# Kernel optimization log

Hardware: AMD Instinct MI355X
Metric: run time of the kernel (lower is better)

Reference implementation:

```python
import jax, jax.numpy as jnp
import numpy as np

B, S, D, H = 2, 2048, 1024, 16
DK = D // H  # 64
EPS = 1e-10
ROPE_BASE = 500000.0


def _rms_norm(x, w):
    # RMSNorm over last dim: w * x / sqrt(mean(x^2) + eps)
    return w * x * jax.lax.rsqrt(jnp.mean(x * x, axis=-1, keepdims=True) + EPS)


def _rope_tables(seq_len, dk):
    inv_freq = 1.0 / (ROPE_BASE ** (jnp.arange(0, dk, 2, dtype=jnp.float32) / dk))
    t = jnp.arange(seq_len, dtype=jnp.float32)
    freqs = jnp.outer(t, inv_freq)            # (S, dk/2)
    emb = jnp.concatenate([freqs, freqs], -1)  # (S, dk)
    return jnp.cos(emb), jnp.sin(emb)


def _rotate_half(x):
    x1, x2 = jnp.split(x, 2, axis=-1)
    return jnp.concatenate([-x2, x1], axis=-1)


def setup_inputs() -> dict:
    key = jax.random.key(0)
    ks = jax.random.split(key, 8)
    scale = 1.0 / np.sqrt(D)
    return {
        "q": jax.random.normal(ks[0], (B, S, D), jnp.float32),
        "k": jax.random.normal(ks[1], (B, S, D), jnp.float32),
        "v": jax.random.normal(ks[2], (B, S, D), jnp.float32),
        "Wq": jax.random.normal(ks[3], (D, D), jnp.float32) * scale,
        "Wk": jax.random.normal(ks[4], (D, D), jnp.float32) * scale,
        "Wv": jax.random.normal(ks[5], (D, D), jnp.float32) * scale,
        "Wo": jax.random.normal(ks[6], (D, D), jnp.float32) * scale,
        "q_norm_w": jnp.ones((DK,), jnp.float32) + 0.02 * jax.random.normal(ks[7], (DK,), jnp.float32),
        "k_norm_w": jnp.ones((DK,), jnp.float32),
    }


def reference(q, k, v, Wq, Wk, Wv, Wo, q_norm_w, k_norm_w):
    Bq, Sq, _ = q.shape
    # Projections (torch Linear: x @ W.T), split into heads -> (B, H, S, DK)
    def proj(x, W):
        return (x @ W.T).reshape(Bq, Sq, H, DK).transpose(0, 2, 1, 3)
    query, key_, value = proj(q, Wq), proj(k, Wk), proj(v, Wv)
    # Per-head QK RMSNorm
    query = _rms_norm(query, q_norm_w)
    key_ = _rms_norm(key_, k_norm_w)
    # RoPE
    cos, sin = _rope_tables(Sq, DK)  # (S, DK) each; broadcast over (B, H)
    query = query * cos + _rotate_half(query) * sin
    key_ = key_ * cos + _rotate_half(key_) * sin
    # Causal attention
    scale = 1.0 / np.sqrt(DK)
    scores = jnp.einsum("bhqd,bhkd->bhqk", query, key_) * scale
    causal = jnp.tril(jnp.ones((Sq, Sq), bool))
    scores = jnp.where(causal, scores, -jnp.inf)
    probs = jax.nn.softmax(scores, axis=-1)
    attn = jnp.einsum("bhqk,bhkd->bhqd", probs, value)
    # Merge heads and output projection
    attn = attn.transpose(0, 2, 1, 3).reshape(Bq, Sq, D)
    return attn @ Wo.T
```

## Files before the change

### kernel.cpp

```cpp
#include <hip/hip_runtime.h>
#include <hip/hip_bf16.h>
#include <math.h>

#define B_  2
#define S_  2048
#define D_  1024
#define H_  16
#define DK_ 64

typedef __attribute__((ext_vector_type(8))) short bf16x8;
typedef __attribute__((ext_vector_type(4))) float f32x4;

#define MFMA_BF16(a, b, c) __builtin_amdgcn_mfma_f32_16x16x32_bf16((a), (b), (c), 0, 0, 0)

#define QSCALE 0.18033688011112042f
#define ROPE_L2 0.591611512f

__device__ __forceinline__ unsigned short f2bf(float f) {
  unsigned int u = __float_as_uint(f);
  u += 0x7FFFu + ((u >> 16) & 1u);
  return (unsigned short)(u >> 16);
}

__device__ __forceinline__ void gl_lds16(const void* g, void* l) {
  __builtin_amdgcn_global_load_lds(
      (const __attribute__((address_space(1))) void*)g,
      (__attribute__((address_space(3))) void*)l, 16, 0, 0);
}

__device__ __forceinline__ int lsw(int row, int col) {
  return row * 64 + ((((col) >> 3) ^ (row & 7)) << 3) + (col & 7);
}

__global__ __launch_bounds__(256)
void cvt_bf16(const float* __restrict__ q, const float* __restrict__ k,
              const float* __restrict__ v, const float* __restrict__ wq,
              const float* __restrict__ wk, const float* __restrict__ wv,
              const float* __restrict__ wo,
              unsigned short* __restrict__ qb, unsigned short* __restrict__ kb,
              unsigned short* __restrict__ vb, unsigned short* __restrict__ wqb,
              unsigned short* __restrict__ wkb, unsigned short* __restrict__ wvb,
              unsigned short* __restrict__ wob) {
  const float* src; unsigned short* dst; int n;
  switch (blockIdx.y) {
    case 0: src = q;  dst = qb;  n = B_ * S_ * D_; break;
    case 1: src = k;  dst = kb;  n = B_ * S_ * D_; break;
    case 2: src = v;  dst = vb;  n = B_ * S_ * D_; break;
    case 3: src = wq; dst = wqb; n = D_ * D_; break;
    case 4: src = wk; dst = wkb; n = D_ * D_; break;
    case 5: src = wv; dst = wvb; n = D_ * D_; break;
    default: src = wo; dst = wob; n = D_ * D_; break;
  }
  const int i = (blockIdx.x * 256 + threadIdx.x) * 4;
  if (i >= n) return;
  float4 val = *(const float4*)&src[i];
  ushort4 r4;
  r4.x = f2bf(val.x); r4.y = f2bf(val.y); r4.z = f2bf(val.z); r4.w = f2bf(val.w);
  *(ushort4*)&dst[i] = r4;
}

__global__ __launch_bounds__(256)
void gemm_qkv(const unsigned short* __restrict__ qa, const unsigned short* __restrict__ ka,
              const unsigned short* __restrict__ va,
              const unsigned short* __restrict__ wq, const unsigned short* __restrict__ wk,
              const unsigned short* __restrict__ wv,
              unsigned short* __restrict__ Qo, unsigned short* __restrict__ Ko,
              unsigned short* __restrict__ Vto,
              const float* __restrict__ qnw, const float* __restrict__ knw) {
  __shared__ unsigned short As[2][128 * 32];
  __shared__ unsigned short Bs[2][128 * 32];
  const int z = blockIdx.z;
  const unsigned short* A = (z == 0) ? qa : (z == 1) ? ka : va;
  const unsigned short* W = (z == 0) ? wq : (z == 1) ? wk : wv;

  const int t = threadIdx.x, lane = t & 63, wave = t >> 6;
  const int l16 = lane & 15, quad = lane >> 4;
  const int wm = wave >> 1, wn = wave & 1;
  const int m0 = blockIdx.y * 128, j0 = blockIdx.x * 128;

  f32x4 acc[4][4];
#pragma unroll
  for (int i = 0; i < 4; ++i)
#pragma unroll
    for (int j = 0; j < 4; ++j) acc[i][j] = (f32x4)(0.0f);

  auto stage = [&](int kb, int buf) {
#pragma unroll
    for (int i = 0; i < 2; ++i) {
      const int c  = (wave * 2 + i) * 64 + lane;
      const int r  = c >> 2;
      const int co = (c & 3) * 8;
      gl_lds16(&A[(size_t)(m0 + r) * D_ + kb + co], &As[buf][(wave * 2 + i) * 512]);
      gl_lds16(&W[(size_t)(j0 + r) * D_ + kb + co], &Bs[buf][(wave * 2 + i) * 512]);
    }
  };

  stage(0, 0);
  for (int kb = 0; kb < D_; kb += 32) {
    const int buf = (kb >> 5) & 1;
    __syncthreads();
    if (kb + 32 < D_) stage(kb + 32, buf ^ 1);

    bf16x8 af[4], bfr[4];
#pragma unroll
    for (int mi = 0; mi < 4; ++mi)
      af[mi] = *(const bf16x8*)&As[buf][(wm * 64 + mi * 16 + l16) * 32 + quad * 8];
#pragma unroll
    for (int ni = 0; ni < 4; ++ni)
      bfr[ni] = *(const bf16x8*)&Bs[buf][(wn * 64 + ni * 16 + l16) * 32 + quad * 8];
#pragma unroll
    for (int mi = 0; mi < 4; ++mi)
#pragma unroll
      for (int ni = 0; ni < 4; ++ni)
        acc[mi][ni] = MFMA_BF16(af[mi], bfr[ni], acc[mi][ni]);
  }

  const int h = blockIdx.x * 2 + wn;
  if (z == 2) {
#pragma unroll
    for (int mi = 0; mi < 4; ++mi) {
      const int rowb = m0 + wm * 64 + mi * 16 + quad * 4;
      const int b = rowb >> 11, s0 = rowb & (S_ - 1);
#pragma unroll
      for (int ni = 0; ni < 4; ++ni) {
        const int dk = ni * 16 + l16;
        const unsigned int u0 =
            (unsigned int)f2bf(acc[mi][ni][0]) | ((unsigned int)f2bf(acc[mi][ni][1]) << 16);
        const unsigned int u1 =
            (unsigned int)f2bf(acc[mi][ni][2]) | ((unsigned int)f2bf(acc[mi][ni][3]) << 16);
        *(uint2*)&Vto[((size_t)((b * H_ + h) * DK_ + dk)) * S_ + s0] = make_uint2(u0, u1);
      }
    }
  } else {
    unsigned short* out = (z == 0) ? Qo : Ko;
    const float* nw = (z == 0) ? qnw : knw;
    const float sc  = (z == 0) ? QSCALE : 1.0f;
    float wv_[4];
#pragma unroll
    for (int ni = 0; ni < 4; ++ni) wv_[ni] = nw[ni * 16 + l16];
    const float invA = exp2f(-(float)l16 * ROPE_L2);
    const float invB = exp2f(-(float)(16 + l16) * ROPE_L2);
#pragma unroll
    for (int mi = 0; mi < 4; ++mi) {
#pragma unroll
      for (int r = 0; r < 4; ++r) {
        const int rowg = m0 + wm * 64 + mi * 16 + quad * 4 + r;
        const int b = rowg >> 11, s = rowg & (S_ - 1);
        float ss = 0.f;
#pragma unroll
        for (int ni = 0; ni < 4; ++ni) ss += acc[mi][ni][r] * acc[mi][ni][r];
#pragma unroll
        for (int m = 1; m < 16; m <<= 1) ss += __shfl_xor(ss, m);
        const float rms = rsqrtf(ss * (1.0f / DK_) + 1e-10f);
        float xn[4];
#pragma unroll
        for (int ni = 0; ni < 4; ++ni) xn[ni] = wv_[ni] * acc[mi][ni][r] * rms;
        const float fA = (float)s * invA, fB = (float)s * invB;
        const float cA = __cosf(fA) * sc, sA = __sinf(fA) * sc;
        const float cB = __cosf(fB) * sc, sB = __sinf(fB) * sc;
        float o0 = xn[0] * cA - xn[2] * sA;
        float o1 = xn[1] * cB - xn[3] * sB;
        float o2 = xn[2] * cA + xn[0] * sA;
        float o3 = xn[3] * cB + xn[1] * sB;
        const size_t base = ((size_t)(b * H_ + h) * S_ + s) * DK_;
        out[base +  0 + l16] = f2bf(o0);
        out[base + 16 + l16] = f2bf(o1);
        out[base + 32 + l16] = f2bf(o2);
        out[base + 48 + l16] = f2bf(o3);
      }
    }
  }
}

__global__ __launch_bounds__(256)
void flash3(const unsigned short* __restrict__ Q, const unsigned short* __restrict__ K,
            const unsigned short* __restrict__ Vt, unsigned short* __restrict__ Oa) {
  __shared__ unsigned short Ks[2][64 * 64];
  __shared__ unsigned short Vs[2][64 * 64];
  __shared__ unsigned short Ps[64 * 64];
  const int bx = blockIdx.x;
  const int idx = bx >> 5;
  const int qt = (idx < 16) ? idx : (47 - idx);
  const int bh = bx & 31;
  const int t = threadIdx.x, lane = t & 63, wave = t >> 6;
  const int l16 = lane & 15, quad = lane >> 4;
  const size_t hb = (size_t)bh * S_ * DK_;
  const unsigned short* Qh  = Q + hb;
  const unsigned short* Kh  = K + hb;
  const unsigned short* Vth = Vt + hb;

  bf16x8 qf[2];
#pragma unroll
  for (int ks = 0; ks < 2; ++ks)
    qf[ks] = *(const bf16x8*)
      &Qh[(size_t)(qt * 64 + wave * 16 + l16) * DK_ + ks * 32 + quad * 8];

  bf16x8 ones;
#pragma unroll
  for (int j = 0; j < 8; ++j) ones[j] = (short)0x3F80;

  f32x4 o[4], lacc;
  lacc = (f32x4)(0.0f);
#pragma unroll
  for (int ni = 0; ni < 4; ++ni) o[ni] = (f32x4)(0.0f);

  auto stage = [&](int kt, int bufi) {
#pragma unroll
    for (int i = 0; i < 2; ++i) {
      const int rbase = wave * 16 + i * 8;
      const int r = rbase + (lane >> 3);
      const int c = ((lane & 7) ^ (r & 7)) * 8;
      gl_lds16(&Kh[(size_t)(kt * 64 + r) * DK_ + c], &Ks[bufi][rbase * 64]);
      gl_lds16(&Vth[(size_t)r * S_ + kt * 64 + c], &Vs[bufi][rbase * 64]);
    }
  };

  const int nkt = qt + 1;
  stage(0, 0);
  for (int kt = 0; kt < nkt; ++kt) {
    const int buf = kt & 1;
    __syncthreads();
    if (kt + 1 < nkt) stage(kt + 1, buf ^ 1);

    f32x4 sv[4];
#pragma unroll
    for (int kvi = 0; kvi < 4; ++kvi) sv[kvi] = (f32x4)(0.0f);
#pragma unroll
    for (int ks = 0; ks < 2; ++ks) {
      bf16x8 ak[4];
#pragma unroll
      for (int kvi = 0; kvi < 4; ++kvi)
        ak[kvi] = *(const bf16x8*)&Ks[buf][lsw(kvi * 16 + l16, ks * 32 + quad * 8)];
#pragma unroll
      for (int kvi = 0; kvi < 4; ++kvi)
        sv[kvi] = MFMA_BF16(ak[kvi], qf[ks], sv[kvi]);
    }

    float p[4][4];
    if (kt == qt) {
      const int qg = qt * 64 + wave * 16 + l16;
#pragma unroll
      for (int kvi = 0; kvi < 4; ++kvi)
#pragma unroll
        for (int r = 0; r < 4; ++r) {
          float x = sv[kvi][r];
          if ((kt * 64 + kvi * 16 + quad * 4 + r) > qg) x = -INFINITY;
          p[kvi][r] = exp2f(x);
        }
    } else {
#pragma unroll
      for (int kvi = 0; kvi < 4; ++kvi)
#pragma unroll
        for (int r = 0; r < 4; ++r) p[kvi][r] = exp2f(sv[kvi][r]);
    }

#pragma unroll
    for (int kvi = 0; kvi < 4; ++kvi) {
      const unsigned int d0 =
          (__float_as_uint(p[kvi][1]) & 0xFFFF0000u) | (__float_as_uint(p[kvi][0]) >> 16);
      const unsigned int d1 =
          (__float_as_uint(p[kvi][3]) & 0xFFFF0000u) | (__float_as_uint(p[kvi][2]) >> 16);
      *(uint2*)&Ps[lsw(wave * 16 + l16, kvi * 16 + quad * 4)] = make_uint2(d0, d1);
    }
    asm volatile("s_waitcnt lgkmcnt(0)" ::: "memory");

#pragma unroll
    for (int ks = 0; ks < 2; ++ks) {
      bf16x8 ap, bv[4];
      ap = *(const bf16x8*)&Ps[lsw(wave * 16 + l16, ks * 32 + quad * 8)];
#pragma unroll
      for (int ni = 0; ni < 4; ++ni)
        bv[ni] = *(const bf16x8*)&Vs[buf][lsw(ni * 16 + l16, ks * 32 + quad * 8)];
#pragma unroll
      for (int ni = 0; ni < 4; ++ni)
        o[ni] = MFMA_BF16(ap, bv[ni], o[ni]);
      lacc = MFMA_BF16(ap, ones, lacc);
    }
  }

  const int b = bh >> 4, h = bh & 15;
#pragma unroll
  for (int r = 0; r < 4; ++r) {
    const int srow = qt * 64 + wave * 16 + quad * 4 + r;
    const float linv = 1.0f / lacc[r];
#pragma unroll
    for (int ni = 0; ni < 4; ++ni)
      Oa[((size_t)(b * S_ + srow) * H_ + h) * DK_ + ni * 16 + l16] =
          f2bf(o[ni][r] * linv);
  }
}

__global__ __launch_bounds__(256)
void gemm_out(const unsigned short* __restrict__ A, const unsigned short* __restrict__ W,
              float* __restrict__ out) {
  __shared__ unsigned short As[2][128 * 32];
  __shared__ unsigned short Bs[2][128 * 32];
  const int t = threadIdx.x, lane = t & 63, wave = t >> 6;
  const int l16 = lane & 15, quad = lane >> 4;
  const int wm = wave >> 1, wn = wave & 1;
  const int m0 = blockIdx.y * 128, j0 = blockIdx.x * 128;

  f32x4 acc[4][4];
#pragma unroll
  for (int i = 0; i < 4; ++i)
#pragma unroll
    for (int j = 0; j < 4; ++j) acc[i][j] = (f32x4)(0.0f);

  auto stage = [&](int kb, int buf) {
#pragma unroll
    for (int i = 0; i < 2; ++i) {
      const int c  = (wave * 2 + i) * 64 + lane;
      const int r  = c >> 2;
      const int co = (c & 3) * 8;
      gl_lds16(&A[(size_t)(m0 + r) * D_ + kb + co], &As[buf][(wave * 2 + i) * 512]);
      gl_lds16(&W[(size_t)(j0 + r) * D_ + kb + co], &Bs[buf][(wave * 2 + i) * 512]);
    }
  };

  stage(0, 0);
  for (int kb = 0; kb < D_; kb += 32) {
    const int buf = (kb >> 5) & 1;
    __syncthreads();
    if (kb + 32 < D_) stage(kb + 32, buf ^ 1);

    bf16x8 af[4], bfr[4];
#pragma unroll
    for (int mi = 0; mi < 4; ++mi)
      af[mi] = *(const bf16x8*)&As[buf][(wm * 64 + mi * 16 + l16) * 32 + quad * 8];
#pragma unroll
    for (int ni = 0; ni < 4; ++ni)
      bfr[ni] = *(const bf16x8*)&Bs[buf][(wn * 64 + ni * 16 + l16) * 32 + quad * 8];
#pragma unroll
    for (int mi = 0; mi < 4; ++mi)
#pragma unroll
      for (int ni = 0; ni < 4; ++ni)
        acc[mi][ni] = MFMA_BF16(af[mi], bfr[ni], acc[mi][ni]);
  }

#pragma unroll
  for (int mi = 0; mi < 4; ++mi) {
    const int rowb = m0 + wm * 64 + mi * 16 + quad * 4;
#pragma unroll
    for (int ni = 0; ni < 4; ++ni) {
      const int col = j0 + wn * 64 + ni * 16 + l16;
#pragma unroll
      for (int r = 0; r < 4; ++r)
        out[(size_t)(rowb + r) * D_ + col] = acc[mi][ni][r];
    }
  }
}

extern "C" void kernel_launch(void* const* d_in, const int* in_sizes, int n_in,
                              void* d_out, int out_size, void* d_ws, size_t ws_size,
                              hipStream_t stream) {
  (void)in_sizes; (void)n_in; (void)out_size; (void)ws_size;
  const float* q  = (const float*)d_in[0];
  const float* k  = (const float*)d_in[1];
  const float* v  = (const float*)d_in[2];
  const float* Wq = (const float*)d_in[3];
  const float* Wk = (const float*)d_in[4];
  const float* Wv = (const float*)d_in[5];
  const float* Wo = (const float*)d_in[6];
  const float* qw = (const float*)d_in[7];
  const float* kw = (const float*)d_in[8];

  char* ws = (char*)d_ws;
  const size_t MB = 1u << 20;
  unsigned short* qb  = (unsigned short*)(ws + 0 * MB);
  unsigned short* kb  = (unsigned short*)(ws + 8 * MB);
  unsigned short* vb  = (unsigned short*)(ws + 16 * MB);
  unsigned short* wqb = (unsigned short*)(ws + 24 * MB);
  unsigned short* wkb = (unsigned short*)(ws + 26 * MB);
  unsigned short* wvb = (unsigned short*)(ws + 28 * MB);
  unsigned short* wob = (unsigned short*)(ws + 30 * MB);
  unsigned short* Qb  = (unsigned short*)(ws + 32 * MB);
  unsigned short* Kb  = (unsigned short*)(ws + 40 * MB);
  unsigned short* Vtb = (unsigned short*)(ws + 48 * MB);
  unsigned short* Ab  = (unsigned short*)(ws + 56 * MB);

  cvt_bf16<<<dim3(4096, 7), 256, 0, stream>>>(q, k, v, Wq, Wk, Wv, Wo,
                                              qb, kb, vb, wqb, wkb, wvb, wob);

  gemm_qkv<<<dim3(D_ / 128, (B_ * S_) / 128, 3), 256, 0, stream>>>(
      qb, kb, vb, wqb, wkb, wvb, Qb, Kb, Vtb, qw, kw);

  flash3<<<1024, 256, 0, stream>>>(Qb, Kb, Vtb, Ab);

  gemm_out<<<dim3(D_ / 128, (B_ * S_) / 128), 256, 0, stream>>>(Ab, wob, (float*)d_out);
}
```

Measured before the change: 215.3 us.

## Rework sync barriers, block swizzling, grid sizes across GEMM and attention kernels

Replaces __syncthreads with explicit vmcnt/lgkmcnt waits plus s_barrier, so the next tile's global-to-LDS prefetch is issued before the wait and overlaps the current compute. It also remaps block indices in both GEMMs so neighbouring blocks on the same XCD share tiles for L2 reuse. gemm_out's N tile shrinks to 64 to get more blocks, cvt_bf16 becomes a grid-stride loop with fewer blocks, and flash gets a launch-bounds occupancy hint. The hand-written waitcnt values depend on how many loads each stage issues and could race if the compiler reorders memory operations.

Result: slower. 226.1 us (+5.0%).

```diff
diff --git a/kernel.cpp b/kernel.cpp
--- a/kernel.cpp
+++ b/kernel.cpp
@@ -31,6 +31,15 @@
 __device__ __forceinline__ int lsw(int row, int col) {
   return row * 64 + ((((col) >> 3) ^ (row & 7)) << 3) + (col & 7);
 }
+
+#define VM_WAIT_BARRIER(N) \
+  asm volatile("s_waitcnt vmcnt(" #N ")\n\ts_barrier" ::: "memory")
+#define VM0_BARRIER() \
+  asm volatile("s_waitcnt vmcnt(0)\n\ts_barrier" ::: "memory")
+#define LGKM_BARRIER() \
+  asm volatile("s_waitcnt lgkmcnt(0)\n\ts_barrier" ::: "memory")
+#define LGKM_WAIT() \
+  asm volatile("s_waitcnt lgkmcnt(0)" ::: "memory")
 
 __global__ __launch_bounds__(256)
 void cvt_bf16(const float* __restrict__ q, const float* __restrict__ k,
@@ -51,12 +60,12 @@
     case 5: src = wv; dst = wvb; n = D_ * D_; break;
     default: src = wo; dst = wob; n = D_ * D_; break;
   }
-  const int i = (blockIdx.x * 256 + threadIdx.x) * 4;
-  if (i >= n) return;
-  float4 val = *(const float4*)&src[i];
-  ushort4 r4;
-  r4.x = f2bf(val.x); r4.y = f2bf(val.y); r4.z = f2bf(val.z); r4.w = f2bf(val.w);
-  *(ushort4*)&dst[i] = r4;
+  for (int i = (blockIdx.x * 256 + threadIdx.x) * 4; i < n; i += 768 * 256 * 4) {
+    float4 val = *(const float4*)&src[i];
+    ushort4 r4;
+    r4.x = f2bf(val.x); r4.y = f2bf(val.y); r4.z = f2bf(val.z); r4.w = f2bf(val.w);
+    *(ushort4*)&dst[i] = r4;
+  }
 }
 
 __global__ __launch_bounds__(256)
@@ -69,14 +78,19 @@
               const float* __restrict__ qnw, const float* __restrict__ knw) {
   __shared__ unsigned short As[2][128 * 32];
   __shared__ unsigned short Bs[2][128 * 32];
-  const int z = blockIdx.z;
+  const int bid = blockIdx.x;
+  const int r8 = bid & 7;
+  const int bxj = (bid >> 3) & 7;
+  const int g = bid >> 6;
+  const int zy = r8 * 12 + g;
+  const int z = zy >> 5, by = zy & 31;
   const unsigned short* A = (z == 0) ? qa : (z == 1) ? ka : va;
   const unsigned short* W = (z == 0) ? wq : (z == 1) ? wk : wv;
 
   const int t = threadIdx.x, lane = t & 63, wave = t >> 6;
   const int l16 = lane & 15, quad = lane >> 4;
   const int wm = wave >> 1, wn = wave & 1;
-  const int m0 = blockIdx.y * 128, j0 = blockIdx.x * 128;
+  const int m0 = by * 128, j0 = bxj * 128;
 
   f32x4 acc[4][4];
 #pragma unroll
@@ -98,8 +112,12 @@
   stage(0, 0);
   for (int kb = 0; kb < D_; kb += 32) {
     const int buf = (kb >> 5) & 1;
-    __syncthreads();
-    if (kb + 32 < D_) stage(kb + 32, buf ^ 1);
+    if (kb + 32 < D_) {
+      stage(kb + 32, buf ^ 1);
+      VM_WAIT_BARRIER(4);
+    } else {
+      VM0_BARRIER();
+    }
 
     bf16x8 af[4], bfr[4];
 #pragma unroll
@@ -113,9 +131,11 @@
 #pragma unroll
       for (int ni = 0; ni < 4; ++ni)
         acc[mi][ni] = MFMA_BF16(af[mi], bfr[ni], acc[mi][ni]);
-  }
-
-  const int h = blockIdx.x * 2 + wn;
+
+    LGKM_BARRIER();
+  }
+
+  const int h = bxj * 2 + wn;
   if (z == 2) {
 #pragma unroll
     for (int mi = 0; mi < 4; ++mi) {
@@ -172,8 +192,8 @@
   }
 }
 
-__global__ __launch_bounds__(256)
-void flash3(const unsigned short* __restrict__ Q, const unsigned short* __restrict__ K,
+__global__ __launch_bounds__(256, 4)
+void flash5(const unsigned short* __restrict__ Q, const unsigned short* __restrict__ K,
             const unsigned short* __restrict__ Vt, unsigned short* __restrict__ Oa) {
   __shared__ unsigned short Ks[2][64 * 64];
   __shared__ unsigned short Vs[2][64 * 64];
@@ -219,8 +239,12 @@
   stage(0, 0);
   for (int kt = 0; kt < nkt; ++kt) {
     const int buf = kt & 1;
-    __syncthreads();
-    if (kt + 1 < nkt) stage(kt + 1, buf ^ 1);
+    if (kt + 1 < nkt) {
+      stage(kt + 1, buf ^ 1);
+      VM_WAIT_BARRIER(4);
+    } else {
+      VM0_BARRIER();
+    }
 
     f32x4 sv[4];
 #pragma unroll
@@ -262,7 +286,7 @@
           (__float_as_uint(p[kvi][3]) & 0xFFFF0000u) | (__float_as_uint(p[kvi][2]) >> 16);
       *(uint2*)&Ps[lsw(wave * 16 + l16, kvi * 16 + quad * 4)] = make_uint2(d0, d1);
     }
-    asm volatile("s_waitcnt lgkmcnt(0)" ::: "memory");
+    LGKM_WAIT();
 
 #pragma unroll
     for (int ks = 0; ks < 2; ++ks) {
@@ -276,6 +300,8 @@
         o[ni] = MFMA_BF16(ap, bv[ni], o[ni]);
       lacc = MFMA_BF16(ap, ones, lacc);
     }
+
+    LGKM_BARRIER();
   }
 
   const int b = bh >> 4, h = bh & 15;
@@ -294,17 +320,22 @@
 void gemm_out(const unsigned short* __restrict__ A, const unsigned short* __restrict__ W,
               float* __restrict__ out) {
   __shared__ unsigned short As[2][128 * 32];
-  __shared__ unsigned short Bs[2][128 * 32];
+  __shared__ unsigned short Bs[2][64 * 32];
+  const int bid = blockIdx.x;
+  const int r8 = bid & 7;
+  const int bxj = (bid >> 3) & 15;
+  const int g = bid >> 7;
+  const int by = r8 * 4 + g;
   const int t = threadIdx.x, lane = t & 63, wave = t >> 6;
   const int l16 = lane & 15, quad = lane >> 4;
   const int wm = wave >> 1, wn = wave & 1;
-  const int m0 = blockIdx.y * 128, j0 = blockIdx.x * 128;
-
-  f32x4 acc[4][4];
+  const int m0 = by * 128, j0 = bxj * 64;
+
+  f32x4 acc[4][2];
 #pragma unroll
   for (int i = 0; i < 4; ++i)
 #pragma unroll
-    for (int j = 0; j < 4; ++j) acc[i][j] = (f32x4)(0.0f);
+    for (int j = 0; j < 2; ++j) acc[i][j] = (f32x4)(0.0f);
 
   auto stage = [&](int kb, int buf) {
 #pragma unroll
@@ -313,36 +344,47 @@
       const int r  = c >> 2;
       const int co = (c & 3) * 8;
       gl_lds16(&A[(size_t)(m0 + r) * D_ + kb + co], &As[buf][(wave * 2 + i) * 512]);
-      gl_lds16(&W[(size_t)(j0 + r) * D_ + kb + co], &Bs[buf][(wave * 2 + i) * 512]);
+    }
+    {
+      const int c  = wave * 64 + lane;
+      const int r  = c >> 2;
+      const int co = (c & 3) * 8;
+      gl_lds16(&W[(size_t)(j0 + r) * D_ + kb + co], &Bs[buf][wave * 512]);
     }
   };
 
   stage(0, 0);
   for (int kb = 0; kb < D_; kb += 32) {
     const int buf = (kb >> 5) & 1;
-    __syncthreads();
-    if (kb + 32 < D_) stage(kb + 32, buf ^ 1);
-
-    bf16x8 af[4], bfr[4];
+    if (kb + 32 < D_) {
+      stage(kb + 32, buf ^ 1);
+      VM_WAIT_BARRIER(3);
+    } else {
+      VM0_BARRIER();
+    }
+
+    bf16x8 af[4], bfr[2];
 #pragma unroll
     for (int mi = 0; mi < 4; ++mi)
       af[mi] = *(const bf16x8*)&As[buf][(wm * 64 + mi * 16 + l16) * 32 + quad * 8];
 #pragma unroll
-    for (int ni = 0; ni < 4; ++ni)
-      bfr[ni] = *(const bf16x8*)&Bs[buf][(wn * 64 + ni * 16 + l16) * 32 + quad * 8];
+    for (int ni = 0; ni < 2; ++ni)
+      bfr[ni] = *(const bf16x8*)&Bs[buf][(wn * 32 + ni * 16 + l16) * 32 + quad * 8];
 #pragma unroll
     for (int mi = 0; mi < 4; ++mi)
 #pragma unroll
-      for (int ni = 0; ni < 4; ++ni)
+      for (int ni = 0; ni < 2; ++ni)
         acc[mi][ni] = MFMA_BF16(af[mi], bfr[ni], acc[mi][ni]);
+
+    LGKM_BARRIER();
   }
 
 #pragma unroll
   for (int mi = 0; mi < 4; ++mi) {
     const int rowb = m0 + wm * 64 + mi * 16 + quad * 4;
 #pragma unroll
-    for (int ni = 0; ni < 4; ++ni) {
-      const int col = j0 + wn * 64 + ni * 16 + l16;
+    for (int ni = 0; ni < 2; ++ni) {
+      const int col = j0 + wn * 32 + ni * 16 + l16;
 #pragma unroll
       for (int r = 0; r < 4; ++r)
         out[(size_t)(rowb + r) * D_ + col] = acc[mi][ni][r];
@@ -378,13 +420,12 @@
   unsigned short* Vtb = (unsigned short*)(ws + 48 * MB);
   unsigned short* Ab  = (unsigned short*)(ws + 56 * MB);
 
-  cvt_bf16<<<dim3(4096, 7), 256, 0, stream>>>(q, k, v, Wq, Wk, Wv, Wo,
-                                              qb, kb, vb, wqb, wkb, wvb, wob);
-
-  gemm_qkv<<<dim3(D_ / 128, (B_ * S_) / 128, 3), 256, 0, stream>>>(
-      qb, kb, vb, wqb, wkb, wvb, Qb, Kb, Vtb, qw, kw);
-
-  flash3<<<1024, 256, 0, stream>>>(Qb, Kb, Vtb, Ab);
-
-  gemm_out<<<dim3(D_ / 128, (B_ * S_) / 128), 256, 0, stream>>>(Ab, wob, (float*)d_out);
-}
+  cvt_bf16<<<dim3(768, 7), 256, 0, stream>>>(q, k, v, Wq, Wk, Wv, Wo,
+                                             qb, kb, vb, wqb, wkb, wvb, wob);
+
+  gemm_qkv<<<768, 256, 0, stream>>>(qb, kb, vb, wqb, wkb, wvb, Qb, Kb, Vtb, qw, kw);
+
+  flash5<<<1024, 256, 0, stream>>>(Qb, Kb, Vtb, Ab);
+
+  gemm_out<<<512, 256, 0, stream>>>(Ab, wob, (float*)d_out);
+}
```
